# Optimization experiments

Hardware: AMD Instinct MI355X
Metric: run time of the kernel (lower is better)

Reference implementation:

```python
import jax, jax.numpy as jnp
import numpy as np

N_NODES = 80000
N_EDGES = 1280000
D_NODE = 128
D_EDGE = 32
HID = 64
OUT = 32
EPS_GEN = 1e-7
EPS_BN = 1e-5


def _lin_init(key, fan_in, fan_out):
    return (jax.random.normal(key, (fan_in, fan_out), jnp.float32) / np.sqrt(fan_in))


def setup_inputs() -> dict:
    key = jax.random.key(0)
    ks = jax.random.split(key, 20)
    inp = {
        "x": jax.random.normal(ks[0], (N_NODES, D_NODE), jnp.float32),
        "edge_index": jax.random.randint(ks[1], (2, N_EDGES), 0, N_NODES, jnp.int32),
        "edge_attr": jax.random.normal(ks[2], (N_EDGES, D_EDGE), jnp.float32),
        # encoders
        "node_W": _lin_init(ks[3], D_NODE, HID), "node_b": jnp.zeros((HID,), jnp.float32),
        "edge_W": _lin_init(ks[4], D_EDGE, HID), "edge_b": jnp.zeros((HID,), jnp.float32),
        # GENConv layer 1 MLP: [HID -> 2HID (bias=False)] -> BN -> ReLU -> [2HID -> HID (bias=False)]
        "c1_W1": _lin_init(ks[5], HID, 2 * HID), "c1_g": jnp.ones((2 * HID,), jnp.float32), "c1_be": jnp.zeros((2 * HID,), jnp.float32), "c1_W2": _lin_init(ks[6], 2 * HID, HID),
        # GENConv layer 2
        "c2_W1": _lin_init(ks[7], HID, 2 * HID), "c2_g": jnp.ones((2 * HID,), jnp.float32), "c2_be": jnp.zeros((2 * HID,), jnp.float32), "c2_W2": _lin_init(ks[8], 2 * HID, HID),
        # edge update linears on concat(3*HID)
        "l1_W": _lin_init(ks[9], 3 * HID, HID), "l1_b": jnp.zeros((HID,), jnp.float32),
        "l2_W": _lin_init(ks[10], 3 * HID, OUT), "l2_b": jnp.zeros((OUT,), jnp.float32),
    }
    return inp


def _scatter_softmax_agg(msg, dst, n_nodes):
    # SoftmaxAggregation with t=1: per-destination, per-feature softmax weights
    m = jax.ops.segment_max(msg, dst, num_segments=n_nodes)  # [N, H]
    m = jnp.where(jnp.isfinite(m), m, 0.0)                   # nodes w/o in-edges
    ex = jnp.exp(msg - m[dst])                               # [E, H]
    denom = jax.ops.segment_sum(ex, dst, num_segments=n_nodes)
    alpha = ex / (denom[dst] + 1e-16)
    return jax.ops.segment_sum(msg * alpha, dst, num_segments=n_nodes)


def _batchnorm(h, gamma, beta):
    mu = jnp.mean(h, axis=0)
    var = jnp.var(h, axis=0)
    return (h - mu) * jax.lax.rsqrt(var + EPS_BN) * gamma + beta


def _genconv(x, src, dst, edge_attr, W1, g, be, W2):
    msg = jax.nn.relu(x[src] + edge_attr) + EPS_GEN          # [E, HID]
    agg = _scatter_softmax_agg(msg, dst, x.shape[0])         # [N, HID]
    h = agg + x
    h = jax.nn.relu(_batchnorm(h @ W1, g, be))
    return h @ W2


def reference(x, edge_index, edge_attr, node_W, node_b, edge_W, edge_b,
              c1_W1, c1_g, c1_be, c1_W2, c2_W1, c2_g, c2_be, c2_W2,
              l1_W, l1_b, l2_W, l2_b):
    src, dst = edge_index[0], edge_index[1]
    ea = edge_attr @ edge_W + edge_b                          # [E, HID]
    h = x @ node_W + node_b                                   # [N, HID]

    convs = [(c1_W1, c1_g, c1_be, c1_W2), (c2_W1, c2_g, c2_be, c2_W2)]
    lins = [(l1_W, l1_b), (l2_W, l2_b)]
    for (W1, g, be, W2), (lW, lb) in zip(convs, lins):
        h = jax.nn.relu(_genconv(h, src, dst, ea, W1, g, be, W2))
        # dropout is identity in eval mode
        ef = jnp.concatenate([h[src], ea, h[dst]], axis=-1)   # [E, 3*HID]
        ea = ef @ lW + lb
    return h, ea
```

## Files before the change

### kernel.cpp

```cpp
#include <hip/hip_runtime.h>
#include <hip/hip_bf16.h>

#define N_NODES 80000
#define N_EDGES 1280000
constexpr int DN = 128;
constexpr int DE = 32;
constexpr int H  = 64;
constexpr int H2 = 128;
constexpr float EPS_GEN = 1e-7f;
constexpr float EPS_BN  = 1e-5f;

typedef _Float16 f16x8 __attribute__((ext_vector_type(8)));
typedef _Float16 f16x4 __attribute__((ext_vector_type(4)));
typedef float f32x4 __attribute__((ext_vector_type(4)));

__device__ __forceinline__ void atomAddF(float* p, float v) {
  __hip_atomic_fetch_add(p, v, __ATOMIC_RELAXED, __HIP_MEMORY_SCOPE_AGENT);
}

__global__ void k_prep_w(const float* __restrict__ W, int K, int OC,
                         _Float16* __restrict__ img) {
  int idx = blockIdx.x * 256 + threadIdx.x;
  int nslabK = K >> 5;
  int j = idx & 7, m16 = (idx >> 3) & 15, kg = (idx >> 7) & 3;
  int slab = idx >> 9;
  int kk = slab % nslabK, n2 = slab / nslabK;
  int k = kk * 32 + kg * 8 + j, n = n2 * 16 + m16;
  img[idx] = (_Float16)W[k * OC + n];
}

template <int K, int OC, bool IN16, bool AFFINE, bool BIAS, bool RELU_OUT, bool OUT16, bool OUT32>
__global__ __launch_bounds__(256) void k_dense(
    const void* __restrict__ Ain, const _Float16* __restrict__ wimg,
    const float* __restrict__ bias, const float* __restrict__ scsh,
    _Float16* __restrict__ out16, float* __restrict__ out32) {
  constexpr int NK = K / 32, NF = OC / 16;
  const int tid = threadIdx.x, wv = tid >> 6, lane = tid & 63;
  const int m16 = lane & 15, kg = lane >> 4;
  const int rowbase = blockIdx.x * 64 + wv * 16;
  f32x4 acc[NF];
#pragma unroll
  for (int n2 = 0; n2 < NF; ++n2) {
    float bv = BIAS ? bias[n2 * 16 + m16] : 0.0f;
    acc[n2] = (f32x4){bv, bv, bv, bv};
  }
  const _Float16* wp = wimg + (size_t)lane * 8;
#pragma unroll
  for (int kk = 0; kk < NK; ++kk) {
    f16x8 a;
    if constexpr (IN16) {
      const _Float16* ap = (const _Float16*)Ain + (size_t)(rowbase + m16) * K + kg * 8 + kk * 32;
      a = *(const f16x8*)ap;
      if constexpr (AFFINE) {
        const float* scp = scsh + kg * 8 + kk * 32;
#pragma unroll
        for (int j = 0; j < 8; ++j) {
          float v = fmaxf(fmaf((float)a[j], scp[j], scp[H2 + j]), 0.0f);
          a[j] = (_Float16)v;
        }
      }
    } else {
      const float* ap = (const float*)Ain + (size_t)(rowbase + m16) * K + kg * 8 + kk * 32;
      float4 v0 = *(const float4*)ap;
      float4 v1 = *(const float4*)(ap + 4);
      a = (f16x8){(_Float16)v0.x, (_Float16)v0.y, (_Float16)v0.z, (_Float16)v0.w,
                  (_Float16)v1.x, (_Float16)v1.y, (_Float16)v1.z, (_Float16)v1.w};
    }
#pragma unroll
    for (int n2 = 0; n2 < NF; ++n2) {
      f16x8 bb = *(const f16x8*)(wp + ((size_t)(n2 * NK + kk) << 9));
      acc[n2] = __builtin_amdgcn_mfma_f32_16x16x32_f16(a, bb, acc[n2], 0, 0, 0);
    }
  }
#pragma unroll
  for (int n2 = 0; n2 < NF; ++n2)
#pragma unroll
    for (int r = 0; r < 4; ++r) {
      float o = acc[n2][r];
      if constexpr (RELU_OUT) o = fmaxf(o, 0.0f);
      size_t oi = (size_t)(rowbase + kg * 4 + r) * OC + n2 * 16 + m16;
      if constexpr (OUT16) out16[oi] = (_Float16)o;
      if constexpr (OUT32) out32[oi] = o;
    }
}

template <int OC, typename OUT_T, int T>
__global__ __launch_bounds__(256) void k_edge_upd_reg(
    const _Float16* __restrict__ h, const _Float16* __restrict__ ea,
    const int* __restrict__ src, const int* __restrict__ dst,
    const _Float16* __restrict__ wimg, const float* __restrict__ lb,
    OUT_T* __restrict__ eout) {
  constexpr int NF = OC / 16;
  __shared__ _Float16 sWf[NF * 6 * 512];
  const int tid = threadIdx.x, wv = tid >> 6, lane = tid & 63;
  const int m16 = lane & 15, kg = lane >> 4;

  {
    const float4* s4 = (const float4*)wimg;
    float4* d4 = (float4*)sWf;
    constexpr int NV = NF * 6 * 512 / 8;
    for (int i = tid; i < NV; i += 256) d4[i] = s4[i];
  }
  __syncthreads();
  const _Float16* wp = sWf + (size_t)lane * 8;

  float bias_[NF];
#pragma unroll
  for (int n2 = 0; n2 < NF; ++n2) bias_[n2] = lb[n2 * 16 + m16];

  const int off = wv * 16 + m16;
  const int t0 = blockIdx.x * T;

  f16x8 FA[6], FB[6];

  auto LOADA = [&](f16x8* F, int row, int s, int d) {
    const _Float16* a0 = h + (size_t)s * H + kg * 8;
    const _Float16* a1 = ea + (size_t)row * H + kg * 8;
    const _Float16* a2 = h + (size_t)d * H + kg * 8;
    F[0] = *(const f16x8*)a0;
    F[1] = *(const f16x8*)(a0 + 32);
    F[2] = *(const f16x8*)a1;
    F[3] = *(const f16x8*)(a1 + 32);
    F[4] = *(const f16x8*)a2;
    F[5] = *(const f16x8*)(a2 + 32);
  };
  auto COMPUTE = [&](const f16x8* F, int row) {
    f32x4 acc[NF];
#pragma unroll
    for (int n2 = 0; n2 < NF; ++n2)
      acc[n2] = (f32x4){bias_[n2], bias_[n2], bias_[n2], bias_[n2]};
#pragma unroll
    for (int kk = 0; kk < 6; ++kk)
#pragma unroll
      for (int n2 = 0; n2 < NF; ++n2) {
        f16x8 bb = *(const f16x8*)(wp + ((n2 * 6 + kk) << 9));
        acc[n2] = __builtin_amdgcn_mfma_f32_16x16x32_f16(F[kk], bb, acc[n2], 0, 0, 0);
      }
    const int rowbase = row - m16;
#pragma unroll
    for (int n2 = 0; n2 < NF; ++n2)
#pragma unroll
      for (int r = 0; r < 4; ++r)
        eout[(size_t)(rowbase + kg * 4 + r) * OC + n2 * 16 + m16] = (OUT_T)acc[n2][r];
  };

  int rA = t0 * 64 + off;
  { int s = src[rA], d = dst[rA]; LOADA(FA, rA, s, d); }
  int rB = rA + 64;
  int sN = src[rB], dN = dst[rB];

#pragma unroll
  for (int i = 0; i < T; i += 2) {
    LOADA(FB, rB, sN, dN);
    int rC = rB + 64, sC = 0, dC = 0;
    if (i + 2 < T) { sC = src[rC]; dC = dst[rC]; }
    COMPUTE(FA, rA);
    if (i + 2 < T) LOADA(FA, rC, sC, dC);
    int rD = rC + 64, sD = 0, dD = 0;
    if (i + 3 < T) { sD = src[rD]; dD = dst[rD]; }
    COMPUTE(FB, rB);
    rA = rC; rB = rD; sN = sD; dN = dD;
  }
}

__global__ void k_hist(const int* __restrict__ dst, int* cnt) {
  int e = blockIdx.x * blockDim.x + threadIdx.x;
  if (e < N_EDGES) atomicAdd(&cnt[dst[e]], 1);
}

__global__ void k_scan_blk(const int* __restrict__ cnt, int* __restrict__ bsum) {
  __shared__ int sh[256];
  int i = blockIdx.x * 256 + threadIdx.x;
  sh[threadIdx.x] = (i < N_NODES) ? cnt[i] : 0;
  __syncthreads();
  for (int s = 128; s > 0; s >>= 1) {
    if (threadIdx.x < s) sh[threadIdx.x] += sh[threadIdx.x + s];
    __syncthreads();
  }
  if (threadIdx.x == 0) bsum[blockIdx.x] = sh[0];
}

__global__ void k_scan_top(int* bsum, int nb) {
  __shared__ int sh[512];
  int t = threadIdx.x;
  int orig = (t < nb) ? bsum[t] : 0;
  sh[t] = orig;
  __syncthreads();
  for (int off = 1; off < 512; off <<= 1) {
    int v = (t >= off) ? sh[t - off] : 0;
    __syncthreads();
    sh[t] += v;
    __syncthreads();
  }
  if (t < nb) bsum[t] = sh[t] - orig;
}

__global__ void k_scan_fin(const int* __restrict__ cnt, const int* __restrict__ bsum,
                           int* __restrict__ start, int* __restrict__ cursor) {
  __shared__ int sh[256];
  int i = blockIdx.x * 256 + threadIdx.x;
  int t = threadIdx.x;
  int orig = (i < N_NODES) ? cnt[i] : 0;
  sh[t] = orig;
  __syncthreads();
  for (int off = 1; off < 256; off <<= 1) {
    int v = (t >= off) ? sh[t - off] : 0;
    __syncthreads();
    sh[t] += v;
    __syncthreads();
  }
  if (i < N_NODES) {
    int st = bsum[blockIdx.x] + sh[t] - orig;
    start[i] = st;
    cursor[i] = st;
  }
}

__global__ void k_scatter(const int* __restrict__ src, const int* __restrict__ dst,
                          int* cursor, int2* __restrict__ eids) {
  int e = blockIdx.x * blockDim.x + threadIdx.x;
  if (e < N_EDGES) {
    int pos = atomicAdd(&cursor[dst[e]], 1);
    eids[pos] = make_int2(e, src[e]);
  }
}

__global__ __launch_bounds__(256) void k_agg_csr(
    const _Float16* __restrict__ h, const _Float16* __restrict__ ea,
    const int2* __restrict__ eids, const int* __restrict__ start,
    const int* __restrict__ cnt, _Float16* __restrict__ hsum) {
  const int lane = threadIdx.x & 63;
  const int wid  = (int)((blockIdx.x * blockDim.x + threadIdx.x) >> 6);
  if (wid >= N_NODES) return;
  const int ep = lane >> 3, fg = lane & 7;
  const int s0 = start[wid], c = cnt[wid];
  float num[8] = {0.f, 0.f, 0.f, 0.f, 0.f, 0.f, 0.f, 0.f};
  float den[8] = {0.f, 0.f, 0.f, 0.f, 0.f, 0.f, 0.f, 0.f};
  if (c > 0) {
    const int nit = (c + 7) >> 3;
    int idx = min(ep, c - 1);
    int2 e = eids[s0 + idx];
    f16x8 hA = *(const f16x8*)(h + (size_t)e.y * H + fg * 8);
    f16x8 eA = *(const f16x8*)(ea + (size_t)e.x * H + fg * 8);
    bool vA = (ep < c);
    f16x8 hB = hA, eB = eA;
    bool vB = false;
    if (nit > 1) {
      idx = min(8 + ep, c - 1);
      e = eids[s0 + idx];
      hB = *(const f16x8*)(h + (size_t)e.y * H + fg * 8);
      eB = *(const f16x8*)(ea + (size_t)e.x * H + fg * 8);
      vB = (8 + ep < c);
    }
    for (int i = 0; i < nit; ++i) {
      f16x8 hc = hA, ec = eA;
      bool vc = vA;
      hA = hB; eA = eB; vA = vB;
      if (i + 2 < nit) {
        idx = min((i + 2) * 8 + ep, c - 1);
        e = eids[s0 + idx];
        hB = *(const f16x8*)(h + (size_t)e.y * H + fg * 8);
        eB = *(const f16x8*)(ea + (size_t)e.x * H + fg * 8);
        vB = ((i + 2) * 8 + ep < c);
      }
#pragma unroll
      for (int j = 0; j < 8; ++j) {
        float m = fmaxf((float)hc[j] + (float)ec[j], 0.0f) + EPS_GEN;
        float ex = vc ? __expf(m) : 0.0f;
        num[j] = fmaf(m, ex, num[j]);
        den[j] += ex;
      }
    }
  }
#pragma unroll
  for (int j = 0; j < 8; ++j) {
    num[j] += __shfl_xor(num[j], 8);
    num[j] += __shfl_xor(num[j], 16);
    num[j] += __shfl_xor(num[j], 32);
    den[j] += __shfl_xor(den[j], 8);
    den[j] += __shfl_xor(den[j], 16);
    den[j] += __shfl_xor(den[j], 32);
  }
  if (ep == 0) {
    f16x8 hs = *(const f16x8*)(h + (size_t)wid * H + fg * 8);
    f16x8 o;
#pragma unroll
    for (int j = 0; j < 8; ++j)
      o[j] = (_Float16)(num[j] / (den[j] + 1e-16f) + (float)hs[j]);
    *(f16x8*)(hsum + (size_t)wid * H + fg * 8) = o;
  }
}

__global__ void k_bnstats(const _Float16* __restrict__ h3, float* sums) {
  int f = threadIdx.x & (H2 - 1);
  int half = threadIdx.x >> 7;
  float s = 0.0f, q = 0.0f;
  for (int n = blockIdx.x * 2 + half; n < N_NODES; n += gridDim.x * 2) {
    float v = (float)h3[(size_t)n * H2 + f];
    s += v;
    q = fmaf(v, v, q);
  }
  __shared__ float sh[2][2][H2];
  sh[0][half][f] = s;
  sh[1][half][f] = q;
  __syncthreads();
  if (threadIdx.x < H2) {
    atomAddF(&sums[f], sh[0][0][f] + sh[0][1][f]);
    atomAddF(&sums[H2 + f], sh[1][0][f] + sh[1][1][f]);
  }
}

__global__ void k_bnfinal(const float* __restrict__ sums, const float* __restrict__ g,
                          const float* __restrict__ be, float* __restrict__ scsh) {
  int f = threadIdx.x;
  if (f < H2) {
    float mu  = sums[f] / (float)N_NODES;
    float var = sums[H2 + f] / (float)N_NODES - mu * mu;
    float sc  = rsqrtf(var + EPS_BN) * g[f];
    scsh[f] = sc;
    scsh[H2 + f] = be[f] - mu * sc;
  }
}

extern "C" void kernel_launch(void* const* d_in, const int* in_sizes, int n_in,
                              void* d_out, int out_size, void* d_ws, size_t ws_size,
                              hipStream_t stream) {
  (void)in_sizes; (void)n_in; (void)out_size; (void)ws_size;
  const float* x      = (const float*)d_in[0];
  const int*   eidx   = (const int*)d_in[1];
  const float* eattr  = (const float*)d_in[2];
  const float* node_W = (const float*)d_in[3];
  const float* node_b = (const float*)d_in[4];
  const float* edge_W = (const float*)d_in[5];
  const float* edge_b = (const float*)d_in[6];
  const float* c1_W1  = (const float*)d_in[7];
  const float* c1_g   = (const float*)d_in[8];
  const float* c1_be  = (const float*)d_in[9];
  const float* c1_W2  = (const float*)d_in[10];
  const float* c2_W1  = (const float*)d_in[11];
  const float* c2_g   = (const float*)d_in[12];
  const float* c2_be  = (const float*)d_in[13];
  const float* c2_W2  = (const float*)d_in[14];
  const float* l1_W   = (const float*)d_in[15];
  const float* l1_b   = (const float*)d_in[16];
  const float* l2_W   = (const float*)d_in[17];
  const float* l2_b   = (const float*)d_in[18];

  const int* src = eidx;
  const int* dst = eidx + N_EDGES;

  char* wsb = (char*)d_ws;
  size_t off = 0;
  _Float16* ea16  = (_Float16*)(wsb + off); off += (size_t)N_EDGES * H * 2;
  _Float16* hA16  = (_Float16*)(wsb + off); off += (size_t)N_NODES * H * 2;
  _Float16* hB16  = (_Float16*)(wsb + off); off += (size_t)N_NODES * H * 2;
  _Float16* hC16  = (_Float16*)(wsb + off); off += (size_t)N_NODES * H * 2;
  _Float16* hsum16= (_Float16*)(wsb + off); off += (size_t)N_NODES * H * 2;
  _Float16* h3    = (_Float16*)(wsb + off); off += (size_t)N_NODES * H2 * 2;
  float* sums     = (float*)(wsb + off);    off += 256 * 4;
  float* scsh     = (float*)(wsb + off);    off += 256 * 4;
  int* cnt        = (int*)(wsb + off);      off += (size_t)N_NODES * 4;
  int* startA     = (int*)(wsb + off);      off += (size_t)N_NODES * 4;
  int* cursor     = (int*)(wsb + off);      off += (size_t)N_NODES * 4;
  int* bsum       = (int*)(wsb + off);      off += 512 * 4;
  int2* eids      = (int2*)(wsb + off);     off += (size_t)N_EDGES * 8;
  _Float16* wE    = (_Float16*)(wsb + off); off += DE * H * 2;
  _Float16* wN    = (_Float16*)(wsb + off); off += DN * H * 2;
  _Float16* w1a   = (_Float16*)(wsb + off); off += H * H2 * 2;
  _Float16* w1b   = (_Float16*)(wsb + off); off += H * H2 * 2;
  _Float16* w2a   = (_Float16*)(wsb + off); off += H2 * H * 2;
  _Float16* w2b   = (_Float16*)(wsb + off); off += H2 * H * 2;
  _Float16* wL1   = (_Float16*)(wsb + off); off += 3 * H * H * 2;
  _Float16* wL2   = (_Float16*)(wsb + off); off += 3 * H * (H / 2) * 2;

  float* h_out  = (float*)d_out;
  float* ea_out = (float*)d_out + (size_t)N_NODES * H;

  constexpr int NB = (N_NODES + 255) / 256;

  k_prep_w<<<DE * H / 256, 256, 0, stream>>>(edge_W, DE, H, wE);
  k_prep_w<<<DN * H / 256, 256, 0, stream>>>(node_W, DN, H, wN);
  k_prep_w<<<H * H2 / 256, 256, 0, stream>>>(c1_W1, H, H2, w1a);
  k_prep_w<<<H * H2 / 256, 256, 0, stream>>>(c2_W1, H, H2, w1b);
  k_prep_w<<<H2 * H / 256, 256, 0, stream>>>(c1_W2, H2, H, w2a);
  k_prep_w<<<H2 * H / 256, 256, 0, stream>>>(c2_W2, H2, H, w2b);
  k_prep_w<<<192 * H / 256, 256, 0, stream>>>(l1_W, 192, H, wL1);
  k_prep_w<<<192 * 32 / 256, 256, 0, stream>>>(l2_W, 192, 32, wL2);

  k_dense<DE, H, false, false, true, false, true, false>
      <<<N_EDGES / 64, 256, 0, stream>>>(eattr, wE, edge_b, nullptr, ea16, nullptr);
  k_dense<DN, H, false, false, true, false, true, false>
      <<<N_NODES / 64, 256, 0, stream>>>(x, wN, node_b, nullptr, hA16, nullptr);

  hipMemsetAsync(cnt, 0, N_NODES * 4, stream);
  k_hist<<<(N_EDGES + 255) / 256, 256, 0, stream>>>(dst, cnt);
  k_scan_blk<<<NB, 256, 0, stream>>>(cnt, bsum);
  k_scan_top<<<1, 512, 0, stream>>>(bsum, NB);
  k_scan_fin<<<NB, 256, 0, stream>>>(cnt, bsum, startA, cursor);
  k_scatter<<<(N_EDGES + 255) / 256, 256, 0, stream>>>(src, dst, cursor, eids);

  hipMemsetAsync(sums, 0, 256 * 4, stream);
  k_agg_csr<<<(N_NODES + 3) / 4, 256, 0, stream>>>(hA16, ea16, eids, startA, cnt, hsum16);
  k_dense<H, H2, true, false, false, false, true, false>
      <<<N_NODES / 64, 256, 0, stream>>>(hsum16, w1a, nullptr, nullptr, h3, nullptr);
  k_bnstats<<<1280, 256, 0, stream>>>(h3, sums);
  k_bnfinal<<<1, 128, 0, stream>>>(sums, c1_g, c1_be, scsh);
  k_dense<H2, H, true, true, false, true, true, false>
      <<<N_NODES / 64, 256, 0, stream>>>(h3, w2a, nullptr, scsh, hB16, nullptr);
  k_edge_upd_reg<64, _Float16, 8>
      <<<N_EDGES / 64 / 8, 256, 0, stream>>>(hB16, ea16, src, dst, wL1, l1_b, ea16);

  hipMemsetAsync(sums, 0, 256 * 4, stream);
  k_agg_csr<<<(N_NODES + 3) / 4, 256, 0, stream>>>(hB16, ea16, eids, startA, cnt, hsum16);
  k_dense<H, H2, true, false, false, false, true, false>
      <<<N_NODES / 64, 256, 0, stream>>>(hsum16, w1b, nullptr, nullptr, h3, nullptr);
  k_bnstats<<<1280, 256, 0, stream>>>(h3, sums);
  k_bnfinal<<<1, 128, 0, stream>>>(sums, c2_g, c2_be, scsh);
  k_dense<H2, H, true, true, false, true, true, true>
      <<<N_NODES / 64, 256, 0, stream>>>(h3, w2b, nullptr, scsh, hC16, h_out);
  k_edge_upd_reg<32, float, 8>
      <<<N_EDGES / 64 / 8, 256, 0, stream>>>(hC16, ea16, src, dst, wL2, l2_b, ea_out);
}
```

Baseline: 729.9 us.

## Store edge features in destination-sorted order and fuse small launches

```diff
diff --git a/kernel.cpp b/kernel.cpp
--- a/kernel.cpp
+++ b/kernel.cpp
@@ -18,26 +18,55 @@
   __hip_atomic_fetch_add(p, v, __ATOMIC_RELAXED, __HIP_MEMORY_SCOPE_AGENT);
 }
 
-__global__ void k_prep_w(const float* __restrict__ W, int K, int OC,
-                         _Float16* __restrict__ img) {
-  int idx = blockIdx.x * 256 + threadIdx.x;
-  int nslabK = K >> 5;
+struct PrepDesc { const float* W; _Float16* img; int K; int OC; int blkStart; };
+struct PrepAll { PrepDesc d[8]; };
+
+__global__ void k_prep_all(PrepAll P) {
+  int b = blockIdx.x;
+  int i = 0;
+#pragma unroll
+  for (int t = 1; t < 8; ++t)
+    if (P.d[t].blkStart <= b) i = t;
+  const PrepDesc D = P.d[i];
+  int idx = (b - D.blkStart) * 256 + threadIdx.x;
+  if (idx >= D.K * D.OC) return;
+  int nslabK = D.K >> 5;
   int j = idx & 7, m16 = (idx >> 3) & 15, kg = (idx >> 7) & 3;
   int slab = idx >> 9;
   int kk = slab % nslabK, n2 = slab / nslabK;
   int k = kk * 32 + kg * 8 + j, n = n2 * 16 + m16;
-  img[idx] = (_Float16)W[k * OC + n];
-}
-
-template <int K, int OC, bool IN16, bool AFFINE, bool BIAS, bool RELU_OUT, bool OUT16, bool OUT32>
+  D.img[idx] = (_Float16)D.W[k * D.OC + n];
+}
+
+template <int K, int OC, bool GATHER, bool IN16, bool AFFINE, bool BIAS,
+          bool RELU_OUT, bool OUT16, bool OUT32, bool CLRS>
 __global__ __launch_bounds__(256) void k_dense(
     const void* __restrict__ Ain, const _Float16* __restrict__ wimg,
-    const float* __restrict__ bias, const float* __restrict__ scsh,
-    _Float16* __restrict__ out16, float* __restrict__ out32) {
+    const float* __restrict__ bias, const float* __restrict__ sums,
+    const float* __restrict__ g, const float* __restrict__ be,
+    const int2* __restrict__ eids,
+    _Float16* __restrict__ out16, float* __restrict__ out32,
+    float* __restrict__ sums_clr) {
   constexpr int NK = K / 32, NF = OC / 16;
+  __shared__ float sSC[H2], sSH[H2];
   const int tid = threadIdx.x, wv = tid >> 6, lane = tid & 63;
   const int m16 = lane & 15, kg = lane >> 4;
   const int rowbase = blockIdx.x * 64 + wv * 16;
+  if constexpr (CLRS) {
+    if (blockIdx.x == 0) sums_clr[tid] = 0.0f;
+  }
+  if constexpr (AFFINE) {
+    for (int i = tid; i < H2; i += 256) {
+      float mu  = sums[i] * (1.0f / N_NODES);
+      float var = sums[H2 + i] * (1.0f / N_NODES) - mu * mu;
+      float sc  = rsqrtf(var + EPS_BN) * g[i];
+      sSC[i] = sc;
+      sSH[i] = be[i] - mu * sc;
+    }
+    __syncthreads();
+  }
+  int arow = rowbase + m16;
+  if constexpr (GATHER) arow = eids[arow].x;
   f32x4 acc[NF];
 #pragma unroll
   for (int n2 = 0; n2 < NF; ++n2) {
@@ -49,18 +78,18 @@
   for (int kk = 0; kk < NK; ++kk) {
     f16x8 a;
     if constexpr (IN16) {
-      const _Float16* ap = (const _Float16*)Ain + (size_t)(rowbase + m16) * K + kg * 8 + kk * 32;
+      const _Float16* ap = (const _Float16*)Ain + (size_t)arow * K + kg * 8 + kk * 32;
       a = *(const f16x8*)ap;
       if constexpr (AFFINE) {
-        const float* scp = scsh + kg * 8 + kk * 32;
 #pragma unroll
         for (int j = 0; j < 8; ++j) {
-          float v = fmaxf(fmaf((float)a[j], scp[j], scp[H2 + j]), 0.0f);
+          int f = kg * 8 + kk * 32 + j;
+          float v = fmaxf(fmaf((float)a[j], sSC[f], sSH[f]), 0.0f);
           a[j] = (_Float16)v;
         }
       }
     } else {
-      const float* ap = (const float*)Ain + (size_t)(rowbase + m16) * K + kg * 8 + kk * 32;
+      const float* ap = (const float*)Ain + (size_t)arow * K + kg * 8 + kk * 32;
       float4 v0 = *(const float4*)ap;
       float4 v1 = *(const float4*)(ap + 4);
       a = (f16x8){(_Float16)v0.x, (_Float16)v0.y, (_Float16)v0.z, (_Float16)v0.w,
@@ -84,17 +113,26 @@
     }
 }
 
-template <int OC, typename OUT_T, int T>
-__global__ __launch_bounds__(256) void k_edge_upd_reg(
+template <int OC, typename OUT_T, int T, bool SCAT>
+__global__ __launch_bounds__(256) void k_edge_upd_srt(
     const _Float16* __restrict__ h, const _Float16* __restrict__ ea,
-    const int* __restrict__ src, const int* __restrict__ dst,
+    const int2* __restrict__ eids, const int* __restrict__ dstS,
     const _Float16* __restrict__ wimg, const float* __restrict__ lb,
     OUT_T* __restrict__ eout) {
   constexpr int NF = OC / 16;
   __shared__ _Float16 sWf[NF * 6 * 512];
+  __shared__ int sS[T * 64], sD[T * 64];
+  __shared__ int sE[SCAT ? T * 64 : 1];
   const int tid = threadIdx.x, wv = tid >> 6, lane = tid & 63;
   const int m16 = lane & 15, kg = lane >> 4;
-
+  const int p0 = blockIdx.x * (T * 64);
+
+  for (int i = tid; i < T * 64; i += 256) {
+    int2 t = eids[p0 + i];
+    sS[i] = t.y;
+    sD[i] = dstS[p0 + i];
+    if constexpr (SCAT) sE[i] = t.x;
+  }
   {
     const float4* s4 = (const float4*)wimg;
     float4* d4 = (float4*)sWf;
@@ -108,15 +146,11 @@
 #pragma unroll
   for (int n2 = 0; n2 < NF; ++n2) bias_[n2] = lb[n2 * 16 + m16];
 
-  const int off = wv * 16 + m16;
-  const int t0 = blockIdx.x * T;
-
   f16x8 FA[6], FB[6];
-
-  auto LOADA = [&](f16x8* F, int row, int s, int d) {
-    const _Float16* a0 = h + (size_t)s * H + kg * 8;
-    const _Float16* a1 = ea + (size_t)row * H + kg * 8;
-    const _Float16* a2 = h + (size_t)d * H + kg * 8;
+  auto LOADA = [&](f16x8* F, int l) {
+    const _Float16* a0 = h + (size_t)sS[l] * H + kg * 8;
+    const _Float16* a1 = ea + (size_t)(p0 + l) * H + kg * 8;
+    const _Float16* a2 = h + (size_t)sD[l] * H + kg * 8;
     F[0] = *(const f16x8*)a0;
     F[1] = *(const f16x8*)(a0 + 32);
     F[2] = *(const f16x8*)a1;
@@ -124,7 +158,7 @@
     F[4] = *(const f16x8*)a2;
     F[5] = *(const f16x8*)(a2 + 32);
   };
-  auto COMPUTE = [&](const f16x8* F, int row) {
+  auto COMPUTE = [&](const f16x8* F, int l) {
     f32x4 acc[NF];
 #pragma unroll
     for (int n2 = 0; n2 < NF; ++n2)
@@ -136,30 +170,32 @@
         f16x8 bb = *(const f16x8*)(wp + ((n2 * 6 + kk) << 9));
         acc[n2] = __builtin_amdgcn_mfma_f32_16x16x32_f16(F[kk], bb, acc[n2], 0, 0, 0);
       }
-    const int rowbase = row - m16;
+    const int lbase = l - m16;
 #pragma unroll
     for (int n2 = 0; n2 < NF; ++n2)
 #pragma unroll
-      for (int r = 0; r < 4; ++r)
-        eout[(size_t)(rowbase + kg * 4 + r) * OC + n2 * 16 + m16] = (OUT_T)acc[n2][r];
+      for (int r = 0; r < 4; ++r) {
+        int lr = lbase + kg * 4 + r;
+        int col = n2 * 16 + m16;
+        if constexpr (SCAT)
+          eout[(size_t)sE[lr] * OC + col] = (OUT_T)acc[n2][r];
+        else
+          eout[(size_t)(p0 + lr) * OC + col] = (OUT_T)acc[n2][r];
+      }
   };
 
-  int rA = t0 * 64 + off;
-  { int s = src[rA], d = dst[rA]; LOADA(FA, rA, s, d); }
-  int rB = rA + 64;
-  int sN = src[rB], dN = dst[rB];
-
-#pragma unroll
-  for (int i = 0; i < T; i += 2) {
-    LOADA(FB, rB, sN, dN);
-    int rC = rB + 64, sC = 0, dC = 0;
-    if (i + 2 < T) { sC = src[rC]; dC = dst[rC]; }
-    COMPUTE(FA, rA);
-    if (i + 2 < T) LOADA(FA, rC, sC, dC);
-    int rD = rC + 64, sD = 0, dD = 0;
-    if (i + 3 < T) { sD = src[rD]; dD = dst[rD]; }
-    COMPUTE(FB, rB);
-    rA = rC; rB = rD; sN = sD; dN = dD;
+  const int l0 = wv * 16 + m16;
+  LOADA(FA, l0);
+  if (T > 1) LOADA(FB, l0 + 64);
+#pragma unroll
+  for (int t = 0; t < T; ++t) {
+    if (t & 1) {
+      COMPUTE(FB, l0 + t * 64);
+      if (t + 2 < T) LOADA(FB, l0 + (t + 2) * 64);
+    } else {
+      COMPUTE(FA, l0 + t * 64);
+      if (t + 2 < T) LOADA(FA, l0 + (t + 2) * 64);
+    }
   }
 }
 
@@ -217,16 +253,18 @@
 }
 
 __global__ void k_scatter(const int* __restrict__ src, const int* __restrict__ dst,
-                          int* cursor, int2* __restrict__ eids) {
+                          int* cursor, int2* __restrict__ eids, int* __restrict__ dstS) {
   int e = blockIdx.x * blockDim.x + threadIdx.x;
   if (e < N_EDGES) {
-    int pos = atomicAdd(&cursor[dst[e]], 1);
+    int d = dst[e];
+    int pos = atomicAdd(&cursor[d], 1);
     eids[pos] = make_int2(e, src[e]);
+    dstS[pos] = d;
   }
 }
 
 __global__ __launch_bounds__(256) void k_agg_csr(
-    const _Float16* __restrict__ h, const _Float16* __restrict__ ea,
+    const _Float16* __restrict__ h, const _Float16* __restrict__ ea_s,
     const int2* __restrict__ eids, const int* __restrict__ start,
     const int* __restrict__ cnt, _Float16* __restrict__ hsum) {
   const int lane = threadIdx.x & 63;
@@ -239,17 +277,15 @@
   if (c > 0) {
     const int nit = (c + 7) >> 3;
     int idx = min(ep, c - 1);
-    int2 e = eids[s0 + idx];
-    f16x8 hA = *(const f16x8*)(h + (size_t)e.y * H + fg * 8);
-    f16x8 eA = *(const f16x8*)(ea + (size_t)e.x * H + fg * 8);
+    f16x8 hA = *(const f16x8*)(h + (size_t)eids[s0 + idx].y * H + fg * 8);
+    f16x8 eA = *(const f16x8*)(ea_s + (size_t)(s0 + idx) * H + fg * 8);
     bool vA = (ep < c);
     f16x8 hB = hA, eB = eA;
     bool vB = false;
     if (nit > 1) {
       idx = min(8 + ep, c - 1);
-      e = eids[s0 + idx];
-      hB = *(const f16x8*)(h + (size_t)e.y * H + fg * 8);
-      eB = *(const f16x8*)(ea + (size_t)e.x * H + fg * 8);
+      hB = *(const f16x8*)(h + (size_t)eids[s0 + idx].y * H + fg * 8);
+      eB = *(const f16x8*)(ea_s + (size_t)(s0 + idx) * H + fg * 8);
       vB = (8 + ep < c);
     }
     for (int i = 0; i < nit; ++i) {
@@ -258,9 +294,8 @@
       hA = hB; eA = eB; vA = vB;
       if (i + 2 < nit) {
         idx = min((i + 2) * 8 + ep, c - 1);
-        e = eids[s0 + idx];
-        hB = *(const f16x8*)(h + (size_t)e.y * H + fg * 8);
-        eB = *(const f16x8*)(ea + (size_t)e.x * H + fg * 8);
+        hB = *(const f16x8*)(h + (size_t)eids[s0 + idx].y * H + fg * 8);
+        eB = *(const f16x8*)(ea_s + (size_t)(s0 + idx) * H + fg * 8);
         vB = ((i + 2) * 8 + ep < c);
       }
 #pragma unroll
@@ -307,18 +342,6 @@
   if (threadIdx.x < H2) {
     atomAddF(&sums[f], sh[0][0][f] + sh[0][1][f]);
     atomAddF(&sums[H2 + f], sh[1][0][f] + sh[1][1][f]);
-  }
-}
-
-__global__ void k_bnfinal(const float* __restrict__ sums, const float* __restrict__ g,
-                          const float* __restrict__ be, float* __restrict__ scsh) {
-  int f = threadIdx.x;
-  if (f < H2) {
-    float mu  = sums[f] / (float)N_NODES;
-    float var = sums[H2 + f] / (float)N_NODES - mu * mu;
-    float sc  = rsqrtf(var + EPS_BN) * g[f];
-    scsh[f] = sc;
-    scsh[H2 + f] = be[f] - mu * sc;
   }
 }
 
@@ -351,19 +374,19 @@
 
   char* wsb = (char*)d_ws;
   size_t off = 0;
-  _Float16* ea16  = (_Float16*)(wsb + off); off += (size_t)N_EDGES * H * 2;
+  _Float16* ea_s  = (_Float16*)(wsb + off); off += (size_t)N_EDGES * H * 2;
   _Float16* hA16  = (_Float16*)(wsb + off); off += (size_t)N_NODES * H * 2;
   _Float16* hB16  = (_Float16*)(wsb + off); off += (size_t)N_NODES * H * 2;
   _Float16* hC16  = (_Float16*)(wsb + off); off += (size_t)N_NODES * H * 2;
   _Float16* hsum16= (_Float16*)(wsb + off); off += (size_t)N_NODES * H * 2;
   _Float16* h3    = (_Float16*)(wsb + off); off += (size_t)N_NODES * H2 * 2;
   float* sums     = (float*)(wsb + off);    off += 256 * 4;
-  float* scsh     = (float*)(wsb + off);    off += 256 * 4;
   int* cnt        = (int*)(wsb + off);      off += (size_t)N_NODES * 4;
   int* startA     = (int*)(wsb + off);      off += (size_t)N_NODES * 4;
   int* cursor     = (int*)(wsb + off);      off += (size_t)N_NODES * 4;
   int* bsum       = (int*)(wsb + off);      off += 512 * 4;
   int2* eids      = (int2*)(wsb + off);     off += (size_t)N_EDGES * 8;
+  int* dstS       = (int*)(wsb + off);      off += (size_t)N_EDGES * 4;
   _Float16* wE    = (_Float16*)(wsb + off); off += DE * H * 2;
   _Float16* wN    = (_Float16*)(wsb + off); off += DN * H * 2;
   _Float16* w1a   = (_Float16*)(wsb + off); off += H * H2 * 2;
@@ -371,53 +394,57 @@
   _Float16* w2a   = (_Float16*)(wsb + off); off += H2 * H * 2;
   _Float16* w2b   = (_Float16*)(wsb + off); off += H2 * H * 2;
   _Float16* wL1   = (_Float16*)(wsb + off); off += 3 * H * H * 2;
-  _Float16* wL2   = (_Float16*)(wsb + off); off += 3 * H * (H / 2) * 2;
+  _Float16* wL2   = (_Float16*)(wsb + off); off += 3 * H * 32 * 2;
 
   float* h_out  = (float*)d_out;
   float* ea_out = (float*)d_out + (size_t)N_NODES * H;
 
   constexpr int NB = (N_NODES + 255) / 256;
 
-  k_prep_w<<<DE * H / 256, 256, 0, stream>>>(edge_W, DE, H, wE);
-  k_prep_w<<<DN * H / 256, 256, 0, stream>>>(node_W, DN, H, wN);
-  k_prep_w<<<H * H2 / 256, 256, 0, stream>>>(c1_W1, H, H2, w1a);
-  k_prep_w<<<H * H2 / 256, 256, 0, stream>>>(c2_W1, H, H2, w1b);
-  k_prep_w<<<H2 * H / 256, 256, 0, stream>>>(c1_W2, H2, H, w2a);
-  k_prep_w<<<H2 * H / 256, 256, 0, stream>>>(c2_W2, H2, H, w2b);
-  k_prep_w<<<192 * H / 256, 256, 0, stream>>>(l1_W, 192, H, wL1);
-  k_prep_w<<<192 * 32 / 256, 256, 0, stream>>>(l2_W, 192, 32, wL2);
-
-  k_dense<DE, H, false, false, true, false, true, false>
-      <<<N_EDGES / 64, 256, 0, stream>>>(eattr, wE, edge_b, nullptr, ea16, nullptr);
-  k_dense<DN, H, false, false, true, false, true, false>
-      <<<N_NODES / 64, 256, 0, stream>>>(x, wN, node_b, nullptr, hA16, nullptr);
+  PrepAll P;
+  P.d[0] = {edge_W, wE, DE, H, 0};
+  P.d[1] = {node_W, wN, DN, H, 8};
+  P.d[2] = {c1_W1, w1a, H, H2, 40};
+  P.d[3] = {c2_W1, w1b, H, H2, 72};
+  P.d[4] = {c1_W2, w2a, H2, H, 104};
+  P.d[5] = {c2_W2, w2b, H2, H, 136};
+  P.d[6] = {l1_W, wL1, 192, H, 168};
+  P.d[7] = {l2_W, wL2, 192, 32, 216};
+  k_prep_all<<<240, 256, 0, stream>>>(P);
 
   hipMemsetAsync(cnt, 0, N_NODES * 4, stream);
   k_hist<<<(N_EDGES + 255) / 256, 256, 0, stream>>>(dst, cnt);
   k_scan_blk<<<NB, 256, 0, stream>>>(cnt, bsum);
   k_scan_top<<<1, 512, 0, stream>>>(bsum, NB);
   k_scan_fin<<<NB, 256, 0, stream>>>(cnt, bsum, startA, cursor);
-  k_scatter<<<(N_EDGES + 255) / 256, 256, 0, stream>>>(src, dst, cursor, eids);
-
-  hipMemsetAsync(sums, 0, 256 * 4, stream);
-  k_agg_csr<<<(N_NODES + 3) / 4, 256, 0, stream>>>(hA16, ea16, eids, startA, cnt, hsum16);
-  k_dense<H, H2, true, false, false, false, true, false>
-      <<<N_NODES / 64, 256, 0, stream>>>(hsum16, w1a, nullptr, nullptr, h3, nullptr);
+  k_scatter<<<(N_EDGES + 255) / 256, 256, 0, stream>>>(src, dst, cursor, eids, dstS);
+
+  k_dense<DE, H, true, false, false, true, false, true, false, false>
+      <<<N_EDGES / 64, 256, 0, stream>>>(eattr, wE, edge_b, nullptr, nullptr, nullptr,
+                                         eids, ea_s, nullptr, nullptr);
+  k_dense<DN, H, false, false, false, true, false, true, false, false>
+      <<<N_NODES / 64, 256, 0, stream>>>(x, wN, node_b, nullptr, nullptr, nullptr,
+                                         nullptr, hA16, nullptr, nullptr);
+
+  k_agg_csr<<<(N_NODES + 3) / 4, 256, 0, stream>>>(hA16, ea_s, eids, startA, cnt, hsum16);
+  k_dense<H, H2, false, true, false, false, false, true, false, true>
+      <<<N_NODES / 64, 256, 0, stream>>>(hsum16, w1a, nullptr, nullptr, nullptr, nullptr,
+                                         nullptr, h3, nullptr, sums);
   k_bnstats<<<1280, 256, 0, stream>>>(h3, sums);
-  k_bnfinal<<<1, 128, 0, stream>>>(sums, c1_g, c1_be, scsh);
-  k_dense<H2, H, true, true, false, true, true, false>
-      <<<N_NODES / 64, 256, 0, stream>>>(h3, w2a, nullptr, scsh, hB16, nullptr);
-  k_edge_upd_reg<64, _Float16, 8>
-      <<<N_EDGES / 64 / 8, 256, 0, stream>>>(hB16, ea16, src, dst, wL1, l1_b, ea16);
-
-  hipMemsetAsync(sums, 0, 256 * 4, stream);
-  k_agg_csr<<<(N_NODES + 3) / 4, 256, 0, stream>>>(hB16, ea16, eids, startA, cnt, hsum16);
-  k_dense<H, H2, true, false, false, false, true, false>
-      <<<N_NODES / 64, 256, 0, stream>>>(hsum16, w1b, nullptr, nullptr, h3, nullptr);
+  k_dense<H2, H, false, true, true, false, true, true, false, false>
+      <<<N_NODES / 64, 256, 0, stream>>>(h3, w2a, nullptr, sums, c1_g, c1_be,
+                                         nullptr, hB16, nullptr, nullptr);
+  k_edge_upd_srt<64, _Float16, 4, false>
+      <<<N_EDGES / 256, 256, 0, stream>>>(hB16, ea_s, eids, dstS, wL1, l1_b, ea_s);
+
+  k_agg_csr<<<(N_NODES + 3) / 4, 256, 0, stream>>>(hB16, ea_s, eids, startA, cnt, hsum16);
+  k_dense<H, H2, false, true, false, false, false, true, false, true>
+      <<<N_NODES / 64, 256, 0, stream>>>(hsum16, w1b, nullptr, nullptr, nullptr, nullptr,
+                                         nullptr, h3, nullptr, sums);
   k_bnstats<<<1280, 256, 0, stream>>>(h3, sums);
-  k_bnfinal<<<1, 128, 0, stream>>>(sums, c2_g, c2_be, scsh);
-  k_dense<H2, H, true, true, false, true, true, true>
-      <<<N_NODES / 64, 256, 0, stream>>>(h3, w2b, nullptr, scsh, hC16, h_out);
-  k_edge_upd_reg<32, float, 8>
-      <<<N_EDGES / 64 / 8, 256, 0, stream>>>(hC16, ea16, src, dst, wL2, l2_b, ea_out);
-}
+  k_dense<H2, H, false, true, true, false, true, true, true, false>
+      <<<N_NODES / 64, 256, 0, stream>>>(h3, w2b, nullptr, sums, c2_g, c2_be,
+                                         nullptr, hC16, h_out, nullptr);
+  k_edge_upd_srt<32, float, 4, true>
+      <<<N_EDGES / 256, 256, 0, stream>>>(hC16, ea_s, eids, dstS, wL2, l2_b, ea_out);
+}
```

After: 686.3 us. 1.06x faster.
